# Kernel tuning notes

Hardware: AMD Instinct MI355X
Metric: run time of the kernel (lower is better)

## Reference

```python
import jax, jax.numpy as jnp
import numpy as np

N = 100000   # nodes
H = 96       # hidden_dim
A = 32       # attn_dim
De = 16      # edge_embeddings_dim
E = 500000   # edges per edge type
NEG_SLOPE = 0.01  # torch F.leaky_relu default


def setup_inputs() -> dict:
    key = jax.random.key(0)
    ks = jax.random.split(key, 24)
    nrm = lambda k, shape, s=1.0: jax.random.normal(k, shape, dtype=jnp.float32) * s
    idx = lambda k: jax.random.randint(k, (E,), 0, N, dtype=jnp.int32)
    Din = 2 * H + De
    return {
        'h': nrm(ks[0], (N, H)),
        'src0': idx(ks[1]), 'dst0': idx(ks[2]),
        'src1': idx(ks[3]), 'dst1': idx(ks[4]),
        'src2': idx(ks[5]), 'dst2': idx(ks[6]),
        'Wm0': nrm(ks[7], (Din, H), Din ** -0.5), 'bm0': jnp.zeros((H,), jnp.float32), 'ef0': nrm(ks[8], (De,)),
        'Wm1': nrm(ks[9], (Din, H), Din ** -0.5), 'bm1': jnp.zeros((H,), jnp.float32), 'ef1': nrm(ks[10], (De,)),
        'Wm2': nrm(ks[11], (Din, H), Din ** -0.5), 'bm2': jnp.zeros((H,), jnp.float32), 'ef2': nrm(ks[12], (De,)),
        'Wn0': nrm(ks[13], (H, A), H ** -0.5), 'Wa0': nrm(ks[14], (2 * A, 1), (2 * A) ** -0.5),
        'Wn1': nrm(ks[15], (H, A), H ** -0.5), 'Wa1': nrm(ks[16], (2 * A, 1), (2 * A) ** -0.5),
        'Wu': nrm(ks[17], (4 * H, H), (4 * H) ** -0.5), 'bu': jnp.zeros((H,), jnp.float32),
    }


def _leaky(x):
    return jnp.where(x > 0, x, NEG_SLOPE * x)


def _edge_msg(h, src, dst, Wm, bm, ef):
    # cat(src_h, dst_h, edge_feature) -> Linear  (dropout p=0, eval mode)
    x = jnp.concatenate([h[src], h[dst], jnp.broadcast_to(ef, (src.shape[0], ef.shape[0]))], axis=-1)
    return x @ Wm + bm  # [E, H]


def _mean_agg(m, dst):
    # fn.mean('m','msg'): per-destination mean over incoming edges
    s = jax.ops.segment_sum(m, dst, num_segments=N)
    c = jax.ops.segment_sum(jnp.ones((m.shape[0],), m.dtype), dst, num_segments=N)
    return s / jnp.maximum(c, 1.0)[:, None]


def _attn_agg(scores, m, dst):
    # per-destination softmax over mailbox (variable-size), then weighted sum
    smax = jax.ops.segment_max(scores, dst, num_segments=N)
    ex = jnp.exp(scores - smax[dst])
    den = jax.ops.segment_sum(ex, dst, num_segments=N)
    num = jax.ops.segment_sum(ex[:, None] * m, dst, num_segments=N)
    return num / jnp.maximum(den, 1e-9)[:, None]


def reference(h, src0, dst0, src1, dst1, src2, dst2,
              Wm0, bm0, ef0, Wm1, bm1, ef1, Wm2, bm2, ef2,
              Wn0, Wa0, Wn1, Wa1, Wu, bu):
    # edge type 0: intra_diff (attention), type 1: inter_diff (attention), type 2: intra_lt (mean)
    m0 = _edge_msg(h, src0, dst0, Wm0, bm0, ef0)
    m1 = _edge_msg(h, src1, dst1, Wm1, bm1, ef1)
    m2 = _edge_msg(h, src2, dst2, Wm2, bm2, ef2)

    z0 = h @ Wn0  # [N, A]
    s0 = _leaky(jnp.concatenate([z0[src0], z0[dst0]], axis=-1) @ Wa0)[:, 0]  # [E]
    z1 = h @ Wn1
    s1 = _leaky(jnp.concatenate([z1[src1], z1[dst1]], axis=-1) @ Wa1)[:, 0]

    msg0 = _attn_agg(s0, m0, dst0)   # [N, H]
    msg1 = _attn_agg(s1, m1, dst1)
    msg2 = _mean_agg(m2, dst2)

    # cross_reducer='stack' then concat over edge-type dim -> [N, 3H]
    mcat = jnp.concatenate([msg0, msg1, msg2], axis=-1)
    # cell node update: Linear(cat(h, m)) + ReLU
    return jax.nn.relu(jnp.concatenate([h, mcat], axis=-1) @ Wu + bu)
```

## Files before the change

kernel.cpp:

```cpp
#include <hip/hip_runtime.h>
#include <hip/hip_bf16.h>
#include <cstdint>

#define NN 100000
#define HH 96
#define AD 32
#define DE 16
#define EE 500000
#define NEG 0.01f

#define GSH 10
#define GSZ 1024
#define KB 98
#define CH 4096
#define BPT 123

typedef __bf16 bf16x8 __attribute__((ext_vector_type(8)));
typedef float  f32x4  __attribute__((ext_vector_type(4)));
typedef unsigned long long ull;

__device__ __forceinline__ unsigned short f2b(float x) {
    union { float f; unsigned int u; } v; v.f = x;
    unsigned int r = v.u + 0x7fffu + ((v.u >> 16) & 1u);
    return (unsigned short)(r >> 16);
}
__device__ __forceinline__ float b2f(unsigned short h) {
    union { unsigned int u; float f; } v; v.u = ((unsigned int)h) << 16;
    return v.f;
}

__global__ void prep_kernel(const float* Wm0, const float* bm0, const float* ef0,
                            const float* Wm1, const float* bm1, const float* ef1,
                            const float* Wm2, const float* bm2, const float* ef2,
                            const float* Wn0, const float* Wa0,
                            const float* Wn1, const float* Wa1,
                            const float* Wu,
                            float* cvec, float* wvec,
                            unsigned short* BfN, unsigned short* BfU) {
    const float* Wm[3] = {Wm0, Wm1, Wm2};
    const float* bm[3] = {bm0, bm1, bm2};
    const float* ef[3] = {ef0, ef1, ef2};
    const int total = 288 + 384 + 55296 + 36864;
    for (int i = blockIdx.x * blockDim.x + threadIdx.x; i < total;
         i += gridDim.x * blockDim.x) {
        if (i < 288) {
            int t = i / 96, j = i % 96;
            float s = bm[t][j];
            for (int k = 0; k < DE; ++k) s += ef[t][k] * Wm[t][(2 * HH + k) * HH + j];
            cvec[i] = s;
        } else if (i < 288 + 384) {
            int ii = i - 288;
            int kind = ii / 96, k = ii % 96;
            const float* Wn = (kind < 2) ? Wn0 : Wn1;
            const float* Wa = (kind < 2) ? Wa0 : Wa1;
            int off = (kind & 1) ? AD : 0;
            float s = 0.f;
            for (int a = 0; a < AD; ++a) s += Wn[k * AD + a] * Wa[off + a];
            wvec[ii] = s;
        } else if (i < 288 + 384 + 55296) {
            int ii = i - 672;
            int sec = ii / 9216; int rem = ii % 9216;
            int ksc = rem / 512; int lj = rem % 512;
            int ks = ksc / 6, c = ksc % 6;
            int lane = lj / 8, jj = lj % 8;
            int quad = lane / 16, m = lane % 16;
            int k = ks * 32 + quad * 8 + jj;
            int n = c * 16 + m;
            int mt = (sec < 3) ? sec : sec - 3;
            int rowoff = (sec < 3) ? 0 : HH;
            BfN[ii] = f2b(Wm[mt][(rowoff + k) * HH + n]);
        } else {
            int ii = i - (672 + 55296);
            int ksc = ii / 512; int lj = ii % 512;
            int ks = ksc / 6, c = ksc % 6;
            int lane = lj / 8, jj = lj % 8;
            int quad = lane / 16, m = lane % 16;
            int k = ks * 32 + quad * 8 + jj;
            int n = c * 16 + m;
            BfU[ii] = f2b(Wu[k * HH + n]);
        }
    }
}

__global__ void cast_uv_kernel(const float* __restrict__ h, const float* __restrict__ wvec,
                               unsigned short* __restrict__ hb, float* __restrict__ uv) {
    int lane = threadIdx.x & 31;
    int node = (blockIdx.x * blockDim.x + threadIdx.x) >> 5;
    if (node >= NN) return;
    float h0 = h[node * HH + lane];
    float h1 = h[node * HH + 32 + lane];
    float h2 = h[node * HH + 64 + lane];
    hb[node * HH + lane] = f2b(h0);
    hb[node * HH + 32 + lane] = f2b(h1);
    hb[node * HH + 64 + lane] = f2b(h2);
    float acc[4];
#pragma unroll
    for (int q = 0; q < 4; ++q)
        acc[q] = h0 * wvec[q * 96 + lane] + h1 * wvec[q * 96 + 32 + lane] +
                 h2 * wvec[q * 96 + 64 + lane];
#pragma unroll
    for (int d = 16; d >= 1; d >>= 1)
#pragma unroll
        for (int q = 0; q < 4; ++q) acc[q] += __shfl_down(acc[q], d, 32);
    if (lane == 0) {
#pragma unroll
        for (int q = 0; q < 4; ++q) uv[q * NN + node] = acc[q];
    }
}

__global__ void zero_kernel(float4* __restrict__ p, int n4) {
    for (int i = blockIdx.x * blockDim.x + threadIdx.x; i < n4;
         i += gridDim.x * blockDim.x)
        p[i] = make_float4(0.f, 0.f, 0.f, 0.f);
}

__global__ void bucket_hist(const int* __restrict__ d0, const int* __restrict__ d1,
                            const int* __restrict__ d2, int* __restrict__ bCnt) {
    __shared__ int hist[3 * KB];
    int t = threadIdx.x;
    for (int j = t; j < 3 * KB; j += 256) hist[j] = 0;
    __syncthreads();
    const int total = 3 * EE;
    for (int i = blockIdx.x * blockDim.x + t; i < total; i += gridDim.x * blockDim.x) {
        int ty = i / EE, e = i - ty * EE;
        const int* d = (ty == 0) ? d0 : (ty == 1) ? d1 : d2;
        atomicAdd(&hist[ty * KB + (d[e] >> GSH)], 1);
    }
    __syncthreads();
    for (int j = t; j < 3 * KB; j += 256)
        if (hist[j]) atomicAdd(&bCnt[j], hist[j]);
}

__global__ void bucket_scan(const int* __restrict__ bCnt, int* __restrict__ bBase,
                            int* __restrict__ gCursor, int* __restrict__ rs,
                            ull* __restrict__ wrec, int* __restrict__ clsCnt) {
    __shared__ int hist[3 * KB];
    int t = threadIdx.x;
    if (t < 3 * KB) hist[t] = bCnt[t];
    if (t < 8) wrec[(size_t)3 * EE + t] = 0ull;
    if (t < 48) clsCnt[t] = 0;
    __syncthreads();
    if (t < 3) {
        int run = 0;
        for (int b = 0; b < KB; ++b) {
            bBase[t * (KB + 1) + b] = run;
            gCursor[t * KB + b] = run;
            run += hist[t * KB + b];
        }
        bBase[t * (KB + 1) + KB] = run;
        rs[(size_t)t * (NN + 1) + NN] = run;
    }
}

__global__ __launch_bounds__(256) void bucket_scatter(
    const int* __restrict__ s0, const int* __restrict__ d0,
    const int* __restrict__ s1, const int* __restrict__ d1,
    const int* __restrict__ s2, const int* __restrict__ d2,
    int* __restrict__ gCursor, unsigned int* __restrict__ binned) {
    __shared__ unsigned int recs[CH];
    __shared__ unsigned short rnk[CH];
    __shared__ unsigned char bkt[CH];
    __shared__ int cnt[KB];
    __shared__ int gpos[KB];
    int t = threadIdx.x;
    int type = blockIdx.x / BPT;
    int chunk = (blockIdx.x % BPT) * CH;
    const int* src = (type == 0) ? s0 : (type == 1) ? s1 : s2;
    const int* dst = (type == 0) ? d0 : (type == 1) ? d1 : d2;
    if (t < KB) cnt[t] = 0;
    __syncthreads();
#pragma unroll
    for (int k = 0; k < CH / 256; ++k) {
        int idx = k * 256 + t;
        int e = chunk + idx;
        if (e < EE) {
            int s = src[e], d = dst[e];
            int b = d >> GSH;
            recs[idx] = ((unsigned int)s << GSH) | (unsigned int)(d & (GSZ - 1));
            bkt[idx] = (unsigned char)b;
            rnk[idx] = (unsigned short)atomicAdd(&cnt[b], 1);
        } else {
            bkt[idx] = 0xFF;
        }
    }
    __syncthreads();
    if (t < KB) {
        int c = cnt[t];
        gpos[t] = (c > 0) ? atomicAdd(&gCursor[type * KB + t], c) : 0;
    }
    __syncthreads();
    unsigned int* bout = binned + (size_t)type * EE;
#pragma unroll
    for (int k = 0; k < CH / 256; ++k) {
        int idx = k * 256 + t;
        unsigned char b = bkt[idx];
        if (b != 0xFF) bout[gpos[b] + rnk[idx]] = recs[idx];
    }
}

__global__ __launch_bounds__(256) void bucket_sort(
    const unsigned int* __restrict__ binned, const int* __restrict__ bBase,
    const float* __restrict__ uv,
    int* __restrict__ rs, ull* __restrict__ wrec, int* __restrict__ clsCnt) {
    __shared__ int cnt[GSZ];
    __shared__ int tsum[256];
    __shared__ float vbuf[GSZ];
    __shared__ int lcls[16];
    int t = threadIdx.x;
    int type = blockIdx.x / KB;
    int b = blockIdx.x % KB;
    int nodeBase = b * GSZ;
    int eb = bBase[type * (KB + 1) + b];
    int en = bBase[type * (KB + 1) + b + 1];
    int n = en - eb;
    const unsigned int* bin = binned + (size_t)type * EE + eb;
#pragma unroll
    for (int k = 0; k < GSZ / 256; ++k) cnt[k * 256 + t] = 0;
    if (t < 16) lcls[t] = 0;
    if (type < 2) {
        const float* vsrc = uv + (2 * type + 1) * NN;
#pragma unroll
        for (int k = 0; k < GSZ / 256; ++k) {
            int nd = nodeBase + k * 256 + t;
            vbuf[k * 256 + t] = (nd < NN) ? vsrc[nd] : 0.f;
        }
    }
    __syncthreads();
    for (int i = t; i < n; i += 256) atomicAdd(&cnt[bin[i] & (GSZ - 1)], 1);
    __syncthreads();
    int v[4], s = 0;
#pragma unroll
    for (int k = 0; k < 4; ++k) { v[k] = cnt[t * 4 + k]; s += v[k]; }
    tsum[t] = s;
    __syncthreads();
    for (int off = 1; off < 256; off <<= 1) {
        int add = (t >= off) ? tsum[t - off] : 0;
        __syncthreads();
        tsum[t] += add;
        __syncthreads();
    }
    int run = tsum[t] - s;
    int offk[4];
#pragma unroll
    for (int k = 0; k < 4; ++k) { offk[k] = run; run += v[k]; }
    int* rsrow = rs + (size_t)type * (NN + 1) + nodeBase;
#pragma unroll
    for (int k = 0; k < 4; ++k) {
        int node = t * 4 + k;
        if (nodeBase + node < NN) {
            rsrow[node] = eb + offk[k];
            int cls = (v[k] + 3) >> 2;
            if (cls > 15) cls = 15;
            atomicAdd(&lcls[cls], 1);
        }
    }
    __syncthreads();
#pragma unroll
    for (int k = 0; k < 4; ++k) cnt[t * 4 + k] = offk[k];
    __syncthreads();
    if (t < 16 && lcls[t]) atomicAdd(&clsCnt[type * 16 + t], lcls[t]);
    ull* wo = wrec + (size_t)type * EE + eb;
    const float* usrc = uv + 2 * type * NN;
    for (int i = t; i < n; i += 256) {
        unsigned int r = bin[i];
        int dl = r & (GSZ - 1);
        int p = atomicAdd(&cnt[dl], 1);
        unsigned int sidx = r >> GSH;
        float w = 1.f;
        if (type < 2) {
            float c = usrc[sidx] + vbuf[dl];
            c = fmaxf(c, NEG * c);
            w = __expf(c);
        }
        wo[p] = ((ull)__float_as_uint(w) << 32) | (ull)(sidx * 192u);
    }
}

__global__ void perm_scan(const int* __restrict__ clsCnt, int* __restrict__ cursor) {
    int t = threadIdx.x;
    if (t < 3) {
        int run = t * NN;
        for (int c = 0; c < 16; ++c) {
            cursor[t * 16 + c] = run;
            run += clsCnt[t * 16 + c];
        }
    }
}

__global__ __launch_bounds__(256) void perm_scatter(const int* __restrict__ rs,
                                                    int* __restrict__ cursor,
                                                    int* __restrict__ perm) {
    __shared__ int lh[48];
    __shared__ int lbase[48];
    int t = threadIdx.x;
    int i = blockIdx.x * 256 + t;
    if (t < 48) lh[t] = 0;
    __syncthreads();
    int cidx = -1, rnkv = 0, node = 0;
    if (i < 3 * NN) {
        int type = i / NN;
        node = i - type * NN;
        const int* r = rs + (size_t)type * (NN + 1) + node;
        int deg = r[1] - r[0];
        int cls = (deg + 3) >> 2;
        if (cls > 15) cls = 15;
        cidx = type * 16 + cls;
        rnkv = atomicAdd(&lh[cidx], 1);
    }
    __syncthreads();
    if (t < 48) lbase[t] = lh[t] ? atomicAdd(&cursor[t], lh[t]) : 0;
    __syncthreads();
    if (cidx >= 0) perm[lbase[cidx] + rnkv] = node;
}

__global__ void aggregate_kernel(const int* __restrict__ rsAll,
                                 const int* __restrict__ perm,
                                 const ull* __restrict__ wrec,
                                 const unsigned short* __restrict__ hb,
                                 unsigned short* __restrict__ hagg,
                                 float* __restrict__ den) {
    const size_t NH = (size_t)NN * HH;
    int lane = threadIdx.x & 31;
    int g = (blockIdx.x * blockDim.x + threadIdx.x) >> 5;
    if (g >= NN) return;
    int t = blockIdx.y;
    int node = perm[t * NN + g];
    const int* rs = rsAll + (size_t)t * (NN + 1);
    const ull* wr = wrec + (size_t)t * EE;
    int beg = rs[node], end = rs[node + 1];
    float a0 = 0.f, a1 = 0.f, a2 = 0.f, dn = 0.f;
    const char* b0 = (const char*)hb + 4 * lane;
    const char* b1 = (const char*)hb + 128 + 2 * lane;
#define EDGE(rec, cond)                                                        \
    {                                                                          \
        float w = (cond) ? __uint_as_float((unsigned int)((rec) >> 32)) : 0.f; \
        unsigned int off = (unsigned int)(rec);                                \
        unsigned int dv = *(const unsigned int*)(b0 + off);                    \
        unsigned int sv = *(const unsigned short*)(b1 + off);                  \
        a0 += w * __uint_as_float(dv << 16);                                   \
        a1 += w * __uint_as_float(dv & 0xFFFF0000u);                           \
        a2 += w * __uint_as_float(sv << 16);                                   \
        dn += w;                                                               \
    }
    for (int j = beg; j < end; j += 4) {
        ull r0 = wr[j], r1 = wr[j + 1], r2 = wr[j + 2], r3 = wr[j + 3];
        EDGE(r0, true);
        EDGE(r1, j + 1 < end);
        EDGE(r2, j + 2 < end);
        EDGE(r3, j + 3 < end);
    }
#undef EDGE
    float inv = (dn > 0.f) ? 1.f / dn : 0.f;
    float q0 = a0 * inv, q1 = a1 * inv, q2 = a2 * inv;
    char* mr = (char*)(hagg + (size_t)t * NH + (size_t)node * HH);
    *(unsigned int*)(mr + 4 * lane) =
        (unsigned int)f2b(q0) | ((unsigned int)f2b(q1) << 16);
    *(unsigned short*)(mr + 128 + 2 * lane) = f2b(q2);
    if (lane == 0) den[(size_t)t * NN + node] = dn;
}

__global__ __launch_bounds__(256) void msg_gemm_kernel(const unsigned short* __restrict__ hagg,
                                                       const unsigned short* __restrict__ hb,
                                                       const unsigned short* __restrict__ BfN,
                                                       const float* __restrict__ den,
                                                       const float* __restrict__ cvec,
                                                       unsigned short* __restrict__ msgb) {
    const size_t NH = (size_t)NN * HH;
    int wave = threadIdx.x >> 6;
    int lane = threadIdx.x & 63;
    int quad = lane >> 4, m = lane & 15;
    int blk = blockIdx.x * 4 + wave;
    if (blk >= NN / 16) return;
    int t = blockIdx.y;
    int r0 = blk * 16;
    const unsigned short* ha = hagg + (size_t)t * NH;
    f32x4 acc[6] = {};
#pragma unroll
    for (int ks = 0; ks < 6; ++ks) {
        const unsigned short* ap =
            (ks < 3) ? ha + (size_t)(r0 + m) * HH + ks * 32 + quad * 8
                     : hb + (size_t)(r0 + m) * HH + (ks - 3) * 32 + quad * 8;
        int sec = (ks < 3) ? t : t + 3;
        int kk = (ks < 3) ? ks : ks - 3;
        bf16x8 af = *(const bf16x8*)ap;
#pragma unroll
        for (int c = 0; c < 6; ++c) {
            bf16x8 bfv = *(const bf16x8*)(BfN + (((sec * 3 + kk) * 6 + c) << 9) + lane * 8);
            acc[c] = __builtin_amdgcn_mfma_f32_16x16x32_bf16(af, bfv, acc[c], 0, 0, 0);
        }
    }
    float dn[4];
#pragma unroll
    for (int r = 0; r < 4; ++r) dn[r] = den[(size_t)t * NN + r0 + quad * 4 + r];
#pragma unroll
    for (int c = 0; c < 6; ++c) {
        float cv = cvec[t * 96 + c * 16 + m];
#pragma unroll
        for (int r = 0; r < 4; ++r) {
            int row = r0 + quad * 4 + r;
            float val = (dn[r] > 0.f) ? (acc[c][r] + cv) : 0.f;
            msgb[(size_t)row * 288 + t * 96 + c * 16 + m] = f2b(val);
        }
    }
}

__global__ __launch_bounds__(256) void update_gemm_kernel(const unsigned short* __restrict__ hb,
                                                          const unsigned short* __restrict__ msgb,
                                                          const unsigned short* __restrict__ BfU,
                                                          const float* __restrict__ bu,
                                                          float* __restrict__ out) {
    int wave = threadIdx.x >> 6;
    int lane = threadIdx.x & 63;
    int quad = lane >> 4, m = lane & 15;
    int blk = blockIdx.x * 4 + wave;
    if (blk >= NN / 16) return;
    int r0 = blk * 16;
    f32x4 acc[6] = {};
#pragma unroll
    for (int ks = 0; ks < 12; ++ks) {
        const unsigned short* ap =
            (ks < 3) ? hb + (size_t)(r0 + m) * HH + ks * 32 + quad * 8
                     : msgb + (size_t)(r0 + m) * 288 + (ks - 3) * 32 + quad * 8;
        bf16x8 af = *(const bf16x8*)ap;
#pragma unroll
        for (int c = 0; c < 6; ++c) {
            bf16x8 bfv = *(const bf16x8*)(BfU + ((ks * 6 + c) << 9) + lane * 8);
            acc[c] = __builtin_amdgcn_mfma_f32_16x16x32_bf16(af, bfv, acc[c], 0, 0, 0);
        }
    }
#pragma unroll
    for (int c = 0; c < 6; ++c) {
        float b = bu[c * 16 + m];
#pragma unroll
        for (int r = 0; r < 4; ++r) {
            int row = r0 + quad * 4 + r;
            float v2 = acc[c][r] + b;
            out[(size_t)row * HH + c * 16 + m] = v2 > 0.f ? v2 : 0.f;
        }
    }
}

extern "C" void kernel_launch(void* const* d_in, const int* in_sizes, int n_in,
                              void* d_out, int out_size, void* d_ws, size_t ws_size,
                              hipStream_t stream) {
    (void)in_sizes; (void)n_in; (void)out_size;
    const float* h   = (const float*)d_in[0];
    const int* srcs[3] = {(const int*)d_in[1], (const int*)d_in[3], (const int*)d_in[5]};
    const int* dsts[3] = {(const int*)d_in[2], (const int*)d_in[4], (const int*)d_in[6]};
    const float* Wm0 = (const float*)d_in[7];
    const float* bm0 = (const float*)d_in[8];
    const float* ef0 = (const float*)d_in[9];
    const float* Wm1 = (const float*)d_in[10];
    const float* bm1 = (const float*)d_in[11];
    const float* ef1 = (const float*)d_in[12];
    const float* Wm2 = (const float*)d_in[13];
    const float* bm2 = (const float*)d_in[14];
    const float* ef2 = (const float*)d_in[15];
    const float* Wn0 = (const float*)d_in[16];
    const float* Wa0 = (const float*)d_in[17];
    const float* Wn1 = (const float*)d_in[18];
    const float* Wa1 = (const float*)d_in[19];
    const float* Wu  = (const float*)d_in[20];
    const float* bu  = (const float*)d_in[21];
    float* out = (float*)d_out;

    const size_t NEED = 157791616;
    if (ws_size < NEED) return;
    char* w = (char*)d_ws;
    unsigned short* msgb    = (unsigned short*)(w + 0);
    unsigned short* hb      = (unsigned short*)(w + 57600000);
    unsigned short* hagg    = (unsigned short*)(w + 76800000);
    float*          den     = (float*)(w + 134400000);
    float*          uv      = (float*)(w + 135600000);
    float*          cvec    = (float*)(w + 137200000);
    float*          wvec    = (float*)(w + 137201280);
    unsigned short* BfN     = (unsigned short*)(w + 137202816);
    unsigned short* BfU     = (unsigned short*)(w + 137313408);
    int*            bBase   = (int*)(w + 137387136);
    int*            gCursor = (int*)(w + 137388416);
    int*            bCnt    = (int*)(w + 137389696);
    int*            rs      = (int*)(w + 137390976);
    ull*            wrec    = (ull*)(w + 138591104);
    unsigned int*   binned  = (unsigned int*)(w + 150591232);
    int*            clsCnt  = (int*)(w + 156591232);
    int*            cursor  = (int*)(w + 156591424);
    int*            perm    = (int*)(w + 156591616);

    prep_kernel<<<128, 256, 0, stream>>>(Wm0, bm0, ef0, Wm1, bm1, ef1, Wm2, bm2, ef2,
                                         Wn0, Wa0, Wn1, Wa1, Wu, cvec, wvec, BfN, BfU);
    cast_uv_kernel<<<12500, 256, 0, stream>>>(h, wvec, hb, uv);

    zero_kernel<<<1, 256, 0, stream>>>((float4*)bCnt, 80);
    bucket_hist<<<512, 256, 0, stream>>>(dsts[0], dsts[1], dsts[2], bCnt);
    bucket_scan<<<1, 384, 0, stream>>>(bCnt, bBase, gCursor, rs, wrec, clsCnt);
    bucket_scatter<<<3 * BPT, 256, 0, stream>>>(srcs[0], dsts[0], srcs[1], dsts[1],
                                                srcs[2], dsts[2], gCursor, binned);
    bucket_sort<<<3 * KB, 256, 0, stream>>>(binned, bBase, uv, rs, wrec, clsCnt);
    perm_scan<<<1, 64, 0, stream>>>(clsCnt, cursor);
    perm_scatter<<<1172, 256, 0, stream>>>(rs, cursor, perm);

    aggregate_kernel<<<dim3(12500, 3), 256, 0, stream>>>(rs, perm, wrec, hb, hagg, den);
    msg_gemm_kernel<<<dim3(1563, 3), 256, 0, stream>>>(hagg, hb, BfN, den, cvec, msgb);
    update_gemm_kernel<<<1563, 256, 0, stream>>>(hb, msgb, BfU, bu, out);
}
```

Before: 342.8 us.

## Pad per-node edge lists to multiples of four and drop degree-class permutation

Each node's CSR segment in the sorted edge-record array is now padded to a multiple of four with zero-weight records, and the offset and padded length are packed into one 64-bit entry. The aggregate kernel then reads the records as aligned 16-byte pairs with no per-edge bounds predicates. It also walks nodes in natural order instead of through a degree-class permutation. This removes the perm_scan and perm_scatter kernels and the class counting in bucket_sort, trading some warp load balance and a larger padded record buffer for fewer launches and simpler inner loops.

```diff
diff --git a/kernel.cpp b/kernel.cpp
--- a/kernel.cpp
+++ b/kernel.cpp
@@ -14,10 +14,12 @@
 #define KB 98
 #define CH 4096
 #define BPT 123
+#define PCAP 801056
 
 typedef __bf16 bf16x8 __attribute__((ext_vector_type(8)));
 typedef float  f32x4  __attribute__((ext_vector_type(4)));
 typedef unsigned long long ull;
+typedef unsigned long long ull2 __attribute__((ext_vector_type(2)));
 
 __device__ __forceinline__ unsigned short f2b(float x) {
     union { float f; unsigned int u; } v; v.f = x;
@@ -132,13 +134,10 @@
 }
 
 __global__ void bucket_scan(const int* __restrict__ bCnt, int* __restrict__ bBase,
-                            int* __restrict__ gCursor, int* __restrict__ rs,
-                            ull* __restrict__ wrec, int* __restrict__ clsCnt) {
+                            int* __restrict__ gCursor) {
     __shared__ int hist[3 * KB];
     int t = threadIdx.x;
     if (t < 3 * KB) hist[t] = bCnt[t];
-    if (t < 8) wrec[(size_t)3 * EE + t] = 0ull;
-    if (t < 48) clsCnt[t] = 0;
     __syncthreads();
     if (t < 3) {
         int run = 0;
@@ -148,7 +147,6 @@
             run += hist[t * KB + b];
         }
         bBase[t * (KB + 1) + KB] = run;
-        rs[(size_t)t * (NN + 1) + NN] = run;
     }
 }
 
@@ -201,11 +199,10 @@
 __global__ __launch_bounds__(256) void bucket_sort(
     const unsigned int* __restrict__ binned, const int* __restrict__ bBase,
     const float* __restrict__ uv,
-    int* __restrict__ rs, ull* __restrict__ wrec, int* __restrict__ clsCnt) {
+    ull* __restrict__ rse, ull* __restrict__ wrec) {
     __shared__ int cnt[GSZ];
     __shared__ int tsum[256];
     __shared__ float vbuf[GSZ];
-    __shared__ int lcls[16];
     int t = threadIdx.x;
     int type = blockIdx.x / KB;
     int b = blockIdx.x % KB;
@@ -213,10 +210,10 @@
     int eb = bBase[type * (KB + 1) + b];
     int en = bBase[type * (KB + 1) + b + 1];
     int n = en - eb;
+    int pbase = eb + 3 * GSZ * b;
     const unsigned int* bin = binned + (size_t)type * EE + eb;
 #pragma unroll
     for (int k = 0; k < GSZ / 256; ++k) cnt[k * 256 + t] = 0;
-    if (t < 16) lcls[t] = 0;
     if (type < 2) {
         const float* vsrc = uv + (2 * type + 1) * NN;
 #pragma unroll
@@ -228,9 +225,13 @@
     __syncthreads();
     for (int i = t; i < n; i += 256) atomicAdd(&cnt[bin[i] & (GSZ - 1)], 1);
     __syncthreads();
-    int v[4], s = 0;
-#pragma unroll
-    for (int k = 0; k < 4; ++k) { v[k] = cnt[t * 4 + k]; s += v[k]; }
+    int v[4], pv[4], s = 0;
+#pragma unroll
+    for (int k = 0; k < 4; ++k) {
+        v[k] = cnt[t * 4 + k];
+        pv[k] = (v[k] + 3) & ~3;
+        s += pv[k];
+    }
     tsum[t] = s;
     __syncthreads();
     for (int off = 1; off < 256; off <<= 1) {
@@ -242,24 +243,21 @@
     int run = tsum[t] - s;
     int offk[4];
 #pragma unroll
-    for (int k = 0; k < 4; ++k) { offk[k] = run; run += v[k]; }
-    int* rsrow = rs + (size_t)type * (NN + 1) + nodeBase;
+    for (int k = 0; k < 4; ++k) { offk[k] = run; run += pv[k]; }
+    ull* wb = wrec + (size_t)type * PCAP;
 #pragma unroll
     for (int k = 0; k < 4; ++k) {
-        int node = t * 4 + k;
-        if (nodeBase + node < NN) {
-            rsrow[node] = eb + offk[k];
-            int cls = (v[k] + 3) >> 2;
-            if (cls > 15) cls = 15;
-            atomicAdd(&lcls[cls], 1);
+        int node = nodeBase + t * 4 + k;
+        if (node < NN) {
+            rse[(size_t)type * NN + node] =
+                ((ull)(unsigned int)pv[k] << 32) | (unsigned int)(pbase + offk[k]);
+            for (int q = v[k]; q < pv[k]; ++q) wb[pbase + offk[k] + q] = 0ull;
         }
     }
     __syncthreads();
 #pragma unroll
     for (int k = 0; k < 4; ++k) cnt[t * 4 + k] = offk[k];
     __syncthreads();
-    if (t < 16 && lcls[t]) atomicAdd(&clsCnt[type * 16 + t], lcls[t]);
-    ull* wo = wrec + (size_t)type * EE + eb;
     const float* usrc = uv + 2 * type * NN;
     for (int i = t; i < n; i += 256) {
         unsigned int r = bin[i];
@@ -272,68 +270,30 @@
             c = fmaxf(c, NEG * c);
             w = __expf(c);
         }
-        wo[p] = ((ull)__float_as_uint(w) << 32) | (ull)(sidx * 192u);
-    }
-}
-
-__global__ void perm_scan(const int* __restrict__ clsCnt, int* __restrict__ cursor) {
-    int t = threadIdx.x;
-    if (t < 3) {
-        int run = t * NN;
-        for (int c = 0; c < 16; ++c) {
-            cursor[t * 16 + c] = run;
-            run += clsCnt[t * 16 + c];
-        }
-    }
-}
-
-__global__ __launch_bounds__(256) void perm_scatter(const int* __restrict__ rs,
-                                                    int* __restrict__ cursor,
-                                                    int* __restrict__ perm) {
-    __shared__ int lh[48];
-    __shared__ int lbase[48];
-    int t = threadIdx.x;
-    int i = blockIdx.x * 256 + t;
-    if (t < 48) lh[t] = 0;
-    __syncthreads();
-    int cidx = -1, rnkv = 0, node = 0;
-    if (i < 3 * NN) {
-        int type = i / NN;
-        node = i - type * NN;
-        const int* r = rs + (size_t)type * (NN + 1) + node;
-        int deg = r[1] - r[0];
-        int cls = (deg + 3) >> 2;
-        if (cls > 15) cls = 15;
-        cidx = type * 16 + cls;
-        rnkv = atomicAdd(&lh[cidx], 1);
-    }
-    __syncthreads();
-    if (t < 48) lbase[t] = lh[t] ? atomicAdd(&cursor[t], lh[t]) : 0;
-    __syncthreads();
-    if (cidx >= 0) perm[lbase[cidx] + rnkv] = node;
-}
-
-__global__ void aggregate_kernel(const int* __restrict__ rsAll,
-                                 const int* __restrict__ perm,
+        wb[pbase + p] = ((ull)__float_as_uint(w) << 32) | (ull)(sidx * 192u);
+    }
+}
+
+__global__ void aggregate_kernel(const ull* __restrict__ rse,
                                  const ull* __restrict__ wrec,
                                  const unsigned short* __restrict__ hb,
                                  unsigned short* __restrict__ hagg,
                                  float* __restrict__ den) {
     const size_t NH = (size_t)NN * HH;
     int lane = threadIdx.x & 31;
-    int g = (blockIdx.x * blockDim.x + threadIdx.x) >> 5;
-    if (g >= NN) return;
+    int node = (blockIdx.x * blockDim.x + threadIdx.x) >> 5;
+    if (node >= NN) return;
     int t = blockIdx.y;
-    int node = perm[t * NN + g];
-    const int* rs = rsAll + (size_t)t * (NN + 1);
-    const ull* wr = wrec + (size_t)t * EE;
-    int beg = rs[node], end = rs[node + 1];
+    ull se = rse[(size_t)t * NN + node];
+    int beg = (int)(unsigned int)se;
+    int end = beg + (int)(se >> 32);
+    const ull* wr = wrec + (size_t)t * PCAP;
     float a0 = 0.f, a1 = 0.f, a2 = 0.f, dn = 0.f;
     const char* b0 = (const char*)hb + 4 * lane;
     const char* b1 = (const char*)hb + 128 + 2 * lane;
-#define EDGE(rec, cond)                                                        \
+#define EDGE(rec)                                                              \
     {                                                                          \
-        float w = (cond) ? __uint_as_float((unsigned int)((rec) >> 32)) : 0.f; \
+        float w = __uint_as_float((unsigned int)((rec) >> 32));                \
         unsigned int off = (unsigned int)(rec);                                \
         unsigned int dv = *(const unsigned int*)(b0 + off);                    \
         unsigned int sv = *(const unsigned short*)(b1 + off);                  \
@@ -343,11 +303,12 @@
         dn += w;                                                               \
     }
     for (int j = beg; j < end; j += 4) {
-        ull r0 = wr[j], r1 = wr[j + 1], r2 = wr[j + 2], r3 = wr[j + 3];
-        EDGE(r0, true);
-        EDGE(r1, j + 1 < end);
-        EDGE(r2, j + 2 < end);
-        EDGE(r3, j + 3 < end);
+        ull2 p0 = *(const ull2*)(wr + j);
+        ull2 p1 = *(const ull2*)(wr + j + 2);
+        EDGE(p0[0]);
+        EDGE(p0[1]);
+        EDGE(p1[0]);
+        EDGE(p1[1]);
     }
 #undef EDGE
     float inv = (dn > 0.f) ? 1.f / dn : 0.f;
@@ -464,7 +425,7 @@
     const float* bu  = (const float*)d_in[21];
     float* out = (float*)d_out;
 
-    const size_t NEED = 157791616;
+    const size_t NEED = 165016320;
     if (ws_size < NEED) return;
     char* w = (char*)d_ws;
     unsigned short* msgb    = (unsigned short*)(w + 0);
@@ -479,12 +440,9 @@
     int*            bBase   = (int*)(w + 137387136);
     int*            gCursor = (int*)(w + 137388416);
     int*            bCnt    = (int*)(w + 137389696);
-    int*            rs      = (int*)(w + 137390976);
-    ull*            wrec    = (ull*)(w + 138591104);
-    unsigned int*   binned  = (unsigned int*)(w + 150591232);
-    int*            clsCnt  = (int*)(w + 156591232);
-    int*            cursor  = (int*)(w + 156591424);
-    int*            perm    = (int*)(w + 156591616);
+    ull*            rse     = (ull*)(w + 137390976);
+    unsigned int*   binned  = (unsigned int*)(w + 139790976);
+    ull*            wrec    = (ull*)(w + 145790976);
 
     prep_kernel<<<128, 256, 0, stream>>>(Wm0, bm0, ef0, Wm1, bm1, ef1, Wm2, bm2, ef2,
                                          Wn0, Wa0, Wn1, Wa1, Wu, cvec, wvec, BfN, BfU);
@@ -492,14 +450,12 @@
 
     zero_kernel<<<1, 256, 0, stream>>>((float4*)bCnt, 80);
     bucket_hist<<<512, 256, 0, stream>>>(dsts[0], dsts[1], dsts[2], bCnt);
-    bucket_scan<<<1, 384, 0, stream>>>(bCnt, bBase, gCursor, rs, wrec, clsCnt);
+    bucket_scan<<<1, 384, 0, stream>>>(bCnt, bBase, gCursor);
     bucket_scatter<<<3 * BPT, 256, 0, stream>>>(srcs[0], dsts[0], srcs[1], dsts[1],
                                                 srcs[2], dsts[2], gCursor, binned);
-    bucket_sort<<<3 * KB, 256, 0, stream>>>(binned, bBase, uv, rs, wrec, clsCnt);
-    perm_scan<<<1, 64, 0, stream>>>(clsCnt, cursor);
-    perm_scatter<<<1172, 256, 0, stream>>>(rs, cursor, perm);
-
-    aggregate_kernel<<<dim3(12500, 3), 256, 0, stream>>>(rs, perm, wrec, hb, hagg, den);
+    bucket_sort<<<3 * KB, 256, 0, stream>>>(binned, bBase, uv, rse, wrec);
+
+    aggregate_kernel<<<dim3(12500, 3), 256, 0, stream>>>(rse, wrec, hb, hagg, den);
     msg_gemm_kernel<<<dim3(1563, 3), 256, 0, stream>>>(hagg, hb, BfN, den, cvec, msgb);
     update_gemm_kernel<<<1563, 256, 0, stream>>>(hb, msgb, BfU, bu, out);
 }
```

Result: faster. 331.2 us (-3.4%).
